# Kernel optimization log

Hardware: AMD Instinct MI355X
Metric: run time of the kernel (lower is better)

## Reference

```python
import jax, jax.numpy as jnp
import numpy as np

TOP_K = 2

def setup_inputs() -> dict:
    key = jax.random.key(0)
    ks = jax.random.split(key, 7)
    B, L, D, H, E, S = 2, 2048, 1024, 512, 16, 2048
    s = lambda fan_in: (1.0 / np.sqrt(fan_in)).astype(np.float32)
    return {
        "x": jax.random.normal(ks[0], (B, L, D), jnp.float32),
        "gate_w": jax.random.normal(ks[1], (E, D), jnp.float32) * s(D),
        "w1": jax.random.normal(ks[2], (E, H, D), jnp.float32) * s(D),
        "w2": jax.random.normal(ks[3], (E, D, H), jnp.float32) * s(H),
        "sfc1": jax.random.normal(ks[4], (S, D), jnp.float32) * s(D),
        "sfc2": jax.random.normal(ks[5], (S, D), jnp.float32) * s(D),
        "sfc3": jax.random.normal(ks[6], (D, S), jnp.float32) * s(S),
    }

def reference(x, gate_w, w1, w2, sfc1, sfc2, sfc3):
    B, L, D = x.shape
    E = gate_w.shape[0]
    # shared expert: SwiGLU MLP
    shared = jnp.einsum("bls,ds->bld", jax.nn.silu(jnp.einsum("bld,sd->bls", x, sfc1)) * jnp.einsum("bld,sd->bls", x, sfc2), sfc3)
    # router: top-k over gate logits, softmax over selected logits only
    logits = jnp.einsum("bld,ed->ble", x, gate_w)
    top_w, top_idx = jax.lax.top_k(logits, TOP_K)           # [B,L,K]
    top_w = jax.nn.softmax(top_w, axis=-1)
    xf = x.reshape(-1, D)                                    # [T,D]
    T = xf.shape[0]
    idx = top_idx.reshape(T, TOP_K)
    wk = top_w.reshape(T, TOP_K)
    # dense combine weights [T,E]: routing weight where selected, else 0
    dispatch = jnp.zeros((T, E), xf.dtype).at[jnp.arange(T)[:, None], idx].add(wk)
    # all-expert dense compute, combined with dispatch weights (avoids [T,E,D])
    h = jax.nn.silu(jnp.einsum("td,ehd->teh", xf, w1))       # [T,E,H]
    moe = jnp.einsum("teh,te,edh->td", h, dispatch, w2)      # [T,D]
    return moe.reshape(B, L, D) + shared
```

## Files before the change

kernel.cpp:

```cpp
#include <hip/hip_runtime.h>
#include <stdint.h>

#define T_TOK 4096
#define D_DIM 1024
#define H_DIM 512
#define E_NUM 16
#define S_DIM 2048

#define DUAL_BLOCKS 512
#define MOE1_TILES_MAX 80
#define SHOUT_BLOCKS 256

typedef __attribute__((ext_vector_type(8))) __bf16 bf16x8;
typedef __attribute__((ext_vector_type(16))) float f32x16;

__device__ __forceinline__ uint16_t f2bf(float f) {
  uint32_t u = __float_as_uint(f);
  u += 0x7fffu + ((u >> 16) & 1u);
  return (uint16_t)(u >> 16);
}

__device__ __forceinline__ float bf2f(uint16_t u) {
  return __uint_as_float(((uint32_t)u) << 16);
}

__device__ __forceinline__ float silu_f(float v) {
  return v / (1.f + __expf(-v));
}

#define N4_X (T_TOK * D_DIM / 4)
#define N4_S (S_DIM * D_DIM / 4)
#define N4_W (E_NUM * H_DIM * D_DIM / 4)
#define N4_TOT (N4_X + 3 * N4_S + 2 * N4_W)
#define N4_GW (E_NUM * D_DIM / 4)

__global__ __launch_bounds__(256) void k_cast_all(
    const float* __restrict__ x, const float* __restrict__ sfc1,
    const float* __restrict__ sfc2, const float* __restrict__ sfc3,
    const float* __restrict__ w1, const float* __restrict__ w2,
    const float* __restrict__ gw,
    uint16_t* __restrict__ xb, uint16_t* __restrict__ s1b,
    uint16_t* __restrict__ s2b, uint16_t* __restrict__ s3b,
    uint16_t* __restrict__ w1b, uint16_t* __restrict__ w2b,
    float4* __restrict__ gwT4) {
  int i = blockIdx.x * 256 + threadIdx.x;
  if (i >= N4_TOT) {
    int t = i - N4_TOT;
    if (t < N4_GW) {
      int k4 = t & (D_DIM / 4 - 1);
      int e = t >> 8;
      gwT4[(size_t)k4 * E_NUM + e] = ((const float4*)(gw + (size_t)e * D_DIM))[k4];
    }
    return;
  }
  const float* src; uint16_t* dst; int off;
  if (i < N4_X)                    { src = x;    dst = xb;  off = 0; }
  else if (i < N4_X + N4_S)        { src = sfc1; dst = s1b; off = N4_X; }
  else if (i < N4_X + 2 * N4_S)    { src = sfc2; dst = s2b; off = N4_X + N4_S; }
  else if (i < N4_X + 3 * N4_S)    { src = sfc3; dst = s3b; off = N4_X + 2 * N4_S; }
  else if (i < N4_X + 3 * N4_S + N4_W) { src = w1; dst = w1b; off = N4_X + 3 * N4_S; }
  else                             { src = w2;  dst = w2b; off = N4_X + 3 * N4_S + N4_W; }
  int j = i - off;
  float4 v = ((const float4*)src)[j];
  ushort4 o;
  o.x = f2bf(v.x); o.y = f2bf(v.y); o.z = f2bf(v.z); o.w = f2bf(v.w);
  ((ushort4*)dst)[j] = o;
}

__global__ __launch_bounds__(256) void k_router(
    const float* __restrict__ x, const float4* __restrict__ gwT4,
    int* __restrict__ top_idx, float* __restrict__ top_w) {
  const int wid = threadIdx.x >> 6, lane = threadIdx.x & 63;
  const int t = blockIdx.x * 4 + wid;
  const int e = lane & 15, q = lane >> 4;
  const float4* xr4 = (const float4*)(x + (size_t)t * D_DIM) + q * 64;
  const float4* g4 = gwT4 + (size_t)q * 64 * E_NUM + e;
  float acc = 0.f;
#pragma unroll 8
  for (int i = 0; i < 64; i++) {
    float4 xv = xr4[i];
    float4 gv = g4[(size_t)i * E_NUM];
    acc += xv.x * gv.x + xv.y * gv.y + xv.z * gv.z + xv.w * gv.w;
  }
  acc += __shfl_xor(acc, 16, 64);
  acc += __shfl_xor(acc, 32, 64);
  float v1 = acc; int i1 = e;
#pragma unroll
  for (int off = 1; off < 16; off <<= 1) {
    float ov = __shfl_xor(v1, off, 64);
    int oi = __shfl_xor(i1, off, 64);
    if (ov > v1 || (ov == v1 && oi < i1)) { v1 = ov; i1 = oi; }
  }
  float v2 = (e == i1) ? -1e30f : acc; int i2 = e;
#pragma unroll
  for (int off = 1; off < 16; off <<= 1) {
    float ov = __shfl_xor(v2, off, 64);
    int oi = __shfl_xor(i2, off, 64);
    if (ov > v2 || (ov == v2 && oi < i2)) { v2 = ov; i2 = oi; }
  }
  if (lane == 0) {
    float w0 = 1.f / (1.f + __expf(v2 - v1));
    top_idx[t * 2] = i1; top_idx[t * 2 + 1] = i2;
    top_w[t * 2] = w0;  top_w[t * 2 + 1] = 1.f - w0;
  }
}

__global__ __launch_bounds__(256) void k_sort(
    const int* __restrict__ top_idx, const float* __restrict__ top_w,
    int* __restrict__ offsets, int* __restrict__ tile_e,
    int* __restrict__ tile_m, int* __restrict__ tile_cnt,
    int* __restrict__ slot_token, float* __restrict__ slot_w,
    int* __restrict__ slot_of) {
  __shared__ int h[E_NUM];
  __shared__ int offs[E_NUM + 1];
  int tid = threadIdx.x;
  if (tid < E_NUM) h[tid] = 0;
  __syncthreads();
  for (int i = tid; i < 2 * T_TOK; i += 256) atomicAdd(&h[top_idx[i]], 1);
  __syncthreads();
  if (tid == 0) {
    int s = 0;
    for (int e = 0; e < E_NUM; e++) { offs[e] = s; s += h[e]; }
    offs[E_NUM] = s;
    int cnt = 0;
    for (int e = 0; e < E_NUM; e++)
      for (int m0 = 0; m0 < h[e]; m0 += 128) { tile_e[cnt] = e; tile_m[cnt] = m0; cnt++; }
    tile_cnt[0] = cnt;
    for (int e = 0; e <= E_NUM; e++) offsets[e] = offs[e];
  }
  __syncthreads();
  if (tid < E_NUM) h[tid] = offs[tid];
  __syncthreads();
  for (int i = tid; i < 2 * T_TOK; i += 256) {
    int e = top_idx[i];
    int slot = atomicAdd(&h[e], 1);
    slot_token[slot] = i >> 1;
    slot_w[slot] = top_w[i];
    slot_of[i] = slot;
  }
}


__global__ __launch_bounds__(256) void k_stage1(
    const uint16_t* __restrict__ xb, const uint16_t* __restrict__ b1,
    const uint16_t* __restrict__ b2, uint16_t* __restrict__ hs,
    const uint16_t* __restrict__ w1b, const int* __restrict__ offsets,
    const int* __restrict__ slot_token, const int* __restrict__ tile_e,
    const int* __restrict__ tile_m, const int* __restrict__ tile_cnt,
    uint16_t* __restrict__ hbuf) {
  __shared__ uint16_t smem[6 * 4096];
  const int bid = blockIdx.x;
  const int tid = threadIdx.x, lane = tid & 63, wid = tid >> 6;
  const int wm = wid >> 1, wn = wid & 1;
  const int m32 = lane & 31, kh = lane >> 5;
  const int row0 = tid >> 2, col8 = (tid & 3) * 8;
  const int st0 = tid * 8, st1 = 2048 + tid * 8;

  if (bid < DUAL_BLOCKS) {
    const int bn0 = (bid & 15) * 128, bm0 = (bid >> 4) * 128;
    uint16_t* sA = smem;
    uint16_t* sB1 = smem + 8192;
    uint16_t* sB2 = smem + 16384;
    f32x16 acc1[2][2], acc2[2][2];
#pragma unroll
    for (int i = 0; i < 2; i++)
#pragma unroll
      for (int j = 0; j < 2; j++) {
        acc1[i][j] = (f32x16)(0.f);
        acc2[i][j] = (f32x16)(0.f);
      }
    const uint16_t* ga0 = xb + (size_t)(bm0 + row0) * D_DIM + col8;
    const uint16_t* ga1 = ga0 + 64 * D_DIM;
    const uint16_t* gb10 = b1 + (size_t)(bn0 + row0) * D_DIM + col8;
    const uint16_t* gb11 = gb10 + 64 * D_DIM;
    const uint16_t* gb20 = b2 + (size_t)(bn0 + row0) * D_DIM + col8;
    const uint16_t* gb21 = gb20 + 64 * D_DIM;

    uint4 pA0, pA1, pB10, pB11, pB20, pB21;
    pA0 = *(const uint4*)ga0;   pA1 = *(const uint4*)ga1;
    pB10 = *(const uint4*)gb10; pB11 = *(const uint4*)gb11;
    pB20 = *(const uint4*)gb20; pB21 = *(const uint4*)gb21;
    ga0 += 32; ga1 += 32; gb10 += 32; gb11 += 32; gb20 += 32; gb21 += 32;
    *(uint4*)(sA + st0) = pA0;   *(uint4*)(sA + st1) = pA1;
    *(uint4*)(sB1 + st0) = pB10; *(uint4*)(sB1 + st1) = pB11;
    *(uint4*)(sB2 + st0) = pB20; *(uint4*)(sB2 + st1) = pB21;
    __syncthreads();

    int cur = 0;
    for (int kt = 32; kt <= D_DIM; kt += 32) {
      if (kt < D_DIM) {
        pA0 = *(const uint4*)ga0;   pA1 = *(const uint4*)ga1;
        pB10 = *(const uint4*)gb10; pB11 = *(const uint4*)gb11;
        pB20 = *(const uint4*)gb20; pB21 = *(const uint4*)gb21;
        ga0 += 32; ga1 += 32; gb10 += 32; gb11 += 32; gb20 += 32; gb21 += 32;
      }
      {
        const uint16_t* A = sA + cur * 4096;
        const uint16_t* B1 = sB1 + cur * 4096;
        const uint16_t* B2 = sB2 + cur * 4096;
#pragma unroll
        for (int ks = 0; ks < 2; ks++) {
          const int ko = ks * 16 + kh * 8;
          bf16x8 a[2], u[2], v[2];
#pragma unroll
          for (int i = 0; i < 2; i++)
            a[i] = *(const bf16x8*)(A + (wm * 64 + i * 32 + m32) * 32 + ko);
#pragma unroll
          for (int j = 0; j < 2; j++) {
            u[j] = *(const bf16x8*)(B1 + (wn * 64 + j * 32 + m32) * 32 + ko);
            v[j] = *(const bf16x8*)(B2 + (wn * 64 + j * 32 + m32) * 32 + ko);
          }
#pragma unroll
          for (int i = 0; i < 2; i++)
#pragma unroll
            for (int j = 0; j < 2; j++) {
              acc1[i][j] = __builtin_amdgcn_mfma_f32_32x32x16_bf16(a[i], u[j], acc1[i][j], 0, 0, 0);
              acc2[i][j] = __builtin_amdgcn_mfma_f32_32x32x16_bf16(a[i], v[j], acc2[i][j], 0, 0, 0);
            }
        }
      }
      if (kt < D_DIM) {
        int nxt = cur ^ 1;
        *(uint4*)(sA + nxt * 4096 + st0) = pA0;   *(uint4*)(sA + nxt * 4096 + st1) = pA1;
        *(uint4*)(sB1 + nxt * 4096 + st0) = pB10; *(uint4*)(sB1 + nxt * 4096 + st1) = pB11;
        *(uint4*)(sB2 + nxt * 4096 + st0) = pB20; *(uint4*)(sB2 + nxt * 4096 + st1) = pB21;
        __syncthreads();
        cur = nxt;
      }
    }
#pragma unroll
    for (int i = 0; i < 2; i++)
#pragma unroll
      for (int j = 0; j < 2; j++)
#pragma unroll
        for (int reg = 0; reg < 16; reg++) {
          int row = bm0 + wm * 64 + i * 32 + (reg & 3) + 8 * (reg >> 2) + 4 * kh;
          int col = bn0 + wn * 64 + j * 32 + m32;
          hs[(size_t)row * S_DIM + col] = f2bf(silu_f(acc1[i][j][reg]) * acc2[i][j][reg]);
        }
  } else {
    int idx = bid - DUAL_BLOCKS;
    int t = idx >> 2;
    if (t >= tile_cnt[0]) return;
    const int n0 = (idx & 3) * 128;
    const int e = tile_e[t], m0 = tile_m[t];
    const int base = offsets[e];
    const int ne = offsets[e + 1] - base;
    uint16_t* sA = smem;
    uint16_t* sB = smem + 8192;
    f32x16 acc[2][2];
#pragma unroll
    for (int i = 0; i < 2; i++)
#pragma unroll
      for (int j = 0; j < 2; j++) acc[i][j] = (f32x16)(0.f);
    const int e0 = min(m0 + row0, ne - 1);
    const int e1 = min(m0 + row0 + 64, ne - 1);
    const uint16_t* ga0 = xb + (size_t)slot_token[base + e0] * D_DIM + col8;
    const uint16_t* ga1 = xb + (size_t)slot_token[base + e1] * D_DIM + col8;
    const uint16_t* wbase = w1b + (size_t)e * H_DIM * D_DIM;
    const uint16_t* gb0 = wbase + (size_t)(n0 + row0) * D_DIM + col8;
    const uint16_t* gb1 = gb0 + 64 * D_DIM;

    uint4 pA0, pA1, pB0, pB1;
    pA0 = *(const uint4*)ga0; pA1 = *(const uint4*)ga1;
    pB0 = *(const uint4*)gb0; pB1 = *(const uint4*)gb1;
    ga0 += 32; ga1 += 32; gb0 += 32; gb1 += 32;
    *(uint4*)(sA + st0) = pA0; *(uint4*)(sA + st1) = pA1;
    *(uint4*)(sB + st0) = pB0; *(uint4*)(sB + st1) = pB1;
    __syncthreads();

    int cur = 0;
    for (int kt = 32; kt <= D_DIM; kt += 32) {
      if (kt < D_DIM) {
        pA0 = *(const uint4*)ga0; pA1 = *(const uint4*)ga1;
        pB0 = *(const uint4*)gb0; pB1 = *(const uint4*)gb1;
        ga0 += 32; ga1 += 32; gb0 += 32; gb1 += 32;
      }
      {
        const uint16_t* A = sA + cur * 4096;
        const uint16_t* B = sB + cur * 4096;
#pragma unroll
        for (int ks = 0; ks < 2; ks++) {
          const int ko = ks * 16 + kh * 8;
          bf16x8 a[2], bb[2];
#pragma unroll
          for (int i = 0; i < 2; i++)
            a[i] = *(const bf16x8*)(A + (wm * 64 + i * 32 + m32) * 32 + ko);
#pragma unroll
          for (int j = 0; j < 2; j++)
            bb[j] = *(const bf16x8*)(B + (wn * 64 + j * 32 + m32) * 32 + ko);
#pragma unroll
          for (int i = 0; i < 2; i++)
#pragma unroll
            for (int j = 0; j < 2; j++)
              acc[i][j] = __builtin_amdgcn_mfma_f32_32x32x16_bf16(a[i], bb[j], acc[i][j], 0, 0, 0);
        }
      }
      if (kt < D_DIM) {
        int nxt = cur ^ 1;
        *(uint4*)(sA + nxt * 4096 + st0) = pA0; *(uint4*)(sA + nxt * 4096 + st1) = pA1;
        *(uint4*)(sB + nxt * 4096 + st0) = pB0; *(uint4*)(sB + nxt * 4096 + st1) = pB1;
        __syncthreads();
        cur = nxt;
      }
    }
#pragma unroll
    for (int i = 0; i < 2; i++)
#pragma unroll
      for (int j = 0; j < 2; j++)
#pragma unroll
        for (int reg = 0; reg < 16; reg++) {
          int ent = m0 + wm * 64 + i * 32 + (reg & 3) + 8 * (reg >> 2) + 4 * kh;
          if (ent < ne) {
            int col = n0 + wn * 64 + j * 32 + m32;
            hbuf[(size_t)(base + ent) * H_DIM + col] = f2bf(silu_f(acc[i][j][reg]));
          }
        }
  }
}

__global__ __launch_bounds__(256) void k_stage2(
    const uint16_t* __restrict__ hsb, const uint16_t* __restrict__ sfc3b,
    float* __restrict__ out, const uint16_t* __restrict__ hbuf,
    const uint16_t* __restrict__ w2b, const int* __restrict__ offsets,
    const float* __restrict__ slot_w, const int* __restrict__ tile_e,
    const int* __restrict__ tile_m, const int* __restrict__ tile_cnt,
    uint16_t* __restrict__ slot_out) {
  __shared__ uint16_t smem[4 * 4096];
  const int bid = blockIdx.x;
  const int tid = threadIdx.x, lane = tid & 63, wid = tid >> 6;
  const int wm = wid >> 1, wn = wid & 1;
  const int m32 = lane & 31, kh = lane >> 5;
  const int row0 = tid >> 2, col8 = (tid & 3) * 8;
  const int st0 = tid * 8, st1 = 2048 + tid * 8;
  uint16_t* sA = smem;
  uint16_t* sB = smem + 8192;

  f32x16 acc[2][2];
#pragma unroll
  for (int i = 0; i < 2; i++)
#pragma unroll
    for (int j = 0; j < 2; j++) acc[i][j] = (f32x16)(0.f);

  const uint16_t *ga0, *ga1, *gb0, *gb1;
  int kiters;
  int bm0 = 0, bn0 = 0, base = 0, ne = 0, m0 = 0, n0 = 0;
  bool is_shout = (bid < SHOUT_BLOCKS);
  if (is_shout) {
    bn0 = (bid & 7) * 128; bm0 = (bid >> 3) * 128;
    ga0 = hsb + (size_t)(bm0 + row0) * S_DIM + col8;
    ga1 = ga0 + (size_t)64 * S_DIM;
    gb0 = sfc3b + (size_t)(bn0 + row0) * S_DIM + col8;
    gb1 = gb0 + (size_t)64 * S_DIM;
    kiters = S_DIM / 32;
  } else {
    int idx = bid - SHOUT_BLOCKS;
    int t = idx >> 3;
    if (t >= tile_cnt[0]) return;
    n0 = (idx & 7) * 128;
    int e = tile_e[t]; m0 = tile_m[t];
    base = offsets[e];
    ne = offsets[e + 1] - base;
    const int e0 = min(m0 + row0, ne - 1);
    const int e1 = min(m0 + row0 + 64, ne - 1);
    ga0 = hbuf + (size_t)(base + e0) * H_DIM + col8;
    ga1 = hbuf + (size_t)(base + e1) * H_DIM + col8;
    const uint16_t* wbase = w2b + (size_t)e * D_DIM * H_DIM;
    gb0 = wbase + (size_t)(n0 + row0) * H_DIM + col8;
    gb1 = gb0 + 64 * H_DIM;
    kiters = H_DIM / 32;
  }

  uint4 pA0, pA1, pB0, pB1;
  pA0 = *(const uint4*)ga0; pA1 = *(const uint4*)ga1;
  pB0 = *(const uint4*)gb0; pB1 = *(const uint4*)gb1;
  ga0 += 32; ga1 += 32; gb0 += 32; gb1 += 32;
  *(uint4*)(sA + st0) = pA0; *(uint4*)(sA + st1) = pA1;
  *(uint4*)(sB + st0) = pB0; *(uint4*)(sB + st1) = pB1;
  __syncthreads();

  int cur = 0;
  for (int kt = 1; kt <= kiters; kt++) {
    if (kt < kiters) {
      pA0 = *(const uint4*)ga0; pA1 = *(const uint4*)ga1;
      pB0 = *(const uint4*)gb0; pB1 = *(const uint4*)gb1;
      ga0 += 32; ga1 += 32; gb0 += 32; gb1 += 32;
    }
    {
      const uint16_t* A = sA + cur * 4096;
      const uint16_t* B = sB + cur * 4096;
#pragma unroll
      for (int ks = 0; ks < 2; ks++) {
        const int ko = ks * 16 + kh * 8;
        bf16x8 a[2], bb[2];
#pragma unroll
        for (int i = 0; i < 2; i++)
          a[i] = *(const bf16x8*)(A + (wm * 64 + i * 32 + m32) * 32 + ko);
#pragma unroll
        for (int j = 0; j < 2; j++)
          bb[j] = *(const bf16x8*)(B + (wn * 64 + j * 32 + m32) * 32 + ko);
#pragma unroll
        for (int i = 0; i < 2; i++)
#pragma unroll
          for (int j = 0; j < 2; j++)
            acc[i][j] = __builtin_amdgcn_mfma_f32_32x32x16_bf16(a[i], bb[j], acc[i][j], 0, 0, 0);
      }
    }
    if (kt < kiters) {
      int nxt = cur ^ 1;
      *(uint4*)(sA + nxt * 4096 + st0) = pA0; *(uint4*)(sA + nxt * 4096 + st1) = pA1;
      *(uint4*)(sB + nxt * 4096 + st0) = pB0; *(uint4*)(sB + nxt * 4096 + st1) = pB1;
      __syncthreads();
      cur = nxt;
    }
  }

  if (is_shout) {
#pragma unroll
    for (int i = 0; i < 2; i++)
#pragma unroll
      for (int j = 0; j < 2; j++)
#pragma unroll
        for (int reg = 0; reg < 16; reg++) {
          int row = bm0 + wm * 64 + i * 32 + (reg & 3) + 8 * (reg >> 2) + 4 * kh;
          int col = bn0 + wn * 64 + j * 32 + m32;
          out[(size_t)row * D_DIM + col] = acc[i][j][reg];
        }
  } else {
#pragma unroll
    for (int i = 0; i < 2; i++)
#pragma unroll
      for (int reg = 0; reg < 16; reg++) {
        int ent = m0 + wm * 64 + i * 32 + (reg & 3) + 8 * (reg >> 2) + 4 * kh;
        if (ent < ne) {
          float w = slot_w[base + ent];
          uint16_t* orow = slot_out + (size_t)(base + ent) * D_DIM;
#pragma unroll
          for (int j = 0; j < 2; j++) {
            int col = n0 + wn * 64 + j * 32 + m32;
            orow[col] = f2bf(w * acc[i][j][reg]);
          }
        }
      }
  }
}

__global__ __launch_bounds__(256) void k_combine(
    const uint16_t* __restrict__ slot_out, const int* __restrict__ slot_of,
    float* __restrict__ out) {
  int t = blockIdx.x;
  int c = threadIdx.x;
  int s0 = slot_of[t * 2], s1 = slot_of[t * 2 + 1];
  ushort4 a = ((const ushort4*)(slot_out + (size_t)s0 * D_DIM))[c];
  ushort4 b = ((const ushort4*)(slot_out + (size_t)s1 * D_DIM))[c];
  float4* po = (float4*)(out + (size_t)t * D_DIM) + c;
  float4 o = *po;
  o.x += bf2f(a.x) + bf2f(b.x);
  o.y += bf2f(a.y) + bf2f(b.y);
  o.z += bf2f(a.z) + bf2f(b.z);
  o.w += bf2f(a.w) + bf2f(b.w);
  *po = o;
}

extern "C" void kernel_launch(void* const* d_in, const int* in_sizes, int n_in,
                              void* d_out, int out_size, void* d_ws, size_t ws_size,
                              hipStream_t stream) {
  const float* x     = (const float*)d_in[0];
  const float* gatew = (const float*)d_in[1];
  const float* w1    = (const float*)d_in[2];
  const float* w2    = (const float*)d_in[3];
  const float* sfc1  = (const float*)d_in[4];
  const float* sfc2  = (const float*)d_in[5];
  const float* sfc3  = (const float*)d_in[6];
  float* out = (float*)d_out;

  uint8_t* ws = (uint8_t*)d_ws;
  size_t off = 0;
  auto alloc = [&](size_t bytes) {
    void* p = ws + off;
    off = (off + bytes + 255) & ~(size_t)255;
    return p;
  };
  uint16_t* xb    = (uint16_t*)alloc((size_t)T_TOK * D_DIM * 2);
  uint16_t* sfc1b = (uint16_t*)alloc((size_t)S_DIM * D_DIM * 2);
  uint16_t* sfc2b = (uint16_t*)alloc((size_t)S_DIM * D_DIM * 2);
  uint16_t* sfc3b = (uint16_t*)alloc((size_t)D_DIM * S_DIM * 2);
  uint16_t* w1b   = (uint16_t*)alloc((size_t)E_NUM * H_DIM * D_DIM * 2);
  uint16_t* w2b   = (uint16_t*)alloc((size_t)E_NUM * D_DIM * H_DIM * 2);
  uint16_t* hsb   = (uint16_t*)alloc((size_t)T_TOK * S_DIM * 2);
  uint16_t* hbuf  = (uint16_t*)alloc((size_t)2 * T_TOK * H_DIM * 2);
  uint16_t* slot_out = (uint16_t*)alloc((size_t)2 * T_TOK * D_DIM * 2);
  float4* gwT4    = (float4*)alloc((size_t)D_DIM / 4 * E_NUM * 16);
  int*   top_idx  = (int*)alloc((size_t)T_TOK * 2 * 4);
  float* top_w    = (float*)alloc((size_t)T_TOK * 2 * 4);
  int*   offsets  = (int*)alloc((E_NUM + 1) * 4);
  int*   tile_e   = (int*)alloc(MOE1_TILES_MAX * 4);
  int*   tile_m   = (int*)alloc(MOE1_TILES_MAX * 4);
  int*   tile_cnt = (int*)alloc(4);
  int*   slot_token = (int*)alloc((size_t)2 * T_TOK * 4);
  float* slot_w   = (float*)alloc((size_t)2 * T_TOK * 4);
  int*   slot_of  = (int*)alloc((size_t)2 * T_TOK * 4);

  k_cast_all<<<(N4_TOT + N4_GW + 255) / 256, 256, 0, stream>>>(
      x, sfc1, sfc2, sfc3, w1, w2, gatew,
      xb, sfc1b, sfc2b, sfc3b, w1b, w2b, gwT4);
  k_router<<<T_TOK / 4, 256, 0, stream>>>(x, gwT4, top_idx, top_w);
  k_sort<<<1, 256, 0, stream>>>(top_idx, top_w, offsets, tile_e, tile_m,
                                tile_cnt, slot_token, slot_w, slot_of);
  k_stage1<<<DUAL_BLOCKS + MOE1_TILES_MAX * 4, 256, 0, stream>>>(
      xb, sfc1b, sfc2b, hsb, w1b, offsets, slot_token, tile_e, tile_m, tile_cnt, hbuf);
  k_stage2<<<SHOUT_BLOCKS + MOE1_TILES_MAX * 8, 256, 0, stream>>>(
      hsb, sfc3b, out, hbuf, w2b, offsets, slot_w, tile_e, tile_m, tile_cnt, slot_out);
  k_combine<<<T_TOK, 256, 0, stream>>>(slot_out, slot_of, out);
}
```

Measured before the change: 354.8 us.

## Switch GEMMs to 16x16x32 MFMA, defer sfc3/w2 casts into stage1, reorder tiles

```diff
diff --git a/kernel.cpp b/kernel.cpp
--- a/kernel.cpp
+++ b/kernel.cpp
@@ -7,12 +7,13 @@
 #define E_NUM 16
 #define S_DIM 2048
 
+#define CAST2_BLOCKS 256
 #define DUAL_BLOCKS 512
 #define MOE1_TILES_MAX 80
 #define SHOUT_BLOCKS 256
 
 typedef __attribute__((ext_vector_type(8))) __bf16 bf16x8;
-typedef __attribute__((ext_vector_type(16))) float f32x16;
+typedef __attribute__((ext_vector_type(4))) float f32x4;
 
 __device__ __forceinline__ uint16_t f2bf(float f) {
   uint32_t u = __float_as_uint(f);
@@ -31,21 +32,20 @@
 #define N4_X (T_TOK * D_DIM / 4)
 #define N4_S (S_DIM * D_DIM / 4)
 #define N4_W (E_NUM * H_DIM * D_DIM / 4)
-#define N4_TOT (N4_X + 3 * N4_S + 2 * N4_W)
+#define N4_P1 (N4_X + 2 * N4_S + N4_W)
 #define N4_GW (E_NUM * D_DIM / 4)
-
-__global__ __launch_bounds__(256) void k_cast_all(
+#define N4_P2 (N4_S + N4_W)
+
+__global__ __launch_bounds__(256) void k_cast1(
     const float* __restrict__ x, const float* __restrict__ sfc1,
-    const float* __restrict__ sfc2, const float* __restrict__ sfc3,
-    const float* __restrict__ w1, const float* __restrict__ w2,
+    const float* __restrict__ sfc2, const float* __restrict__ w1,
     const float* __restrict__ gw,
     uint16_t* __restrict__ xb, uint16_t* __restrict__ s1b,
-    uint16_t* __restrict__ s2b, uint16_t* __restrict__ s3b,
-    uint16_t* __restrict__ w1b, uint16_t* __restrict__ w2b,
+    uint16_t* __restrict__ s2b, uint16_t* __restrict__ w1b,
     float4* __restrict__ gwT4) {
   int i = blockIdx.x * 256 + threadIdx.x;
-  if (i >= N4_TOT) {
-    int t = i - N4_TOT;
+  if (i >= N4_P1) {
+    int t = i - N4_P1;
     if (t < N4_GW) {
       int k4 = t & (D_DIM / 4 - 1);
       int e = t >> 8;
@@ -54,12 +54,10 @@
     return;
   }
   const float* src; uint16_t* dst; int off;
-  if (i < N4_X)                    { src = x;    dst = xb;  off = 0; }
-  else if (i < N4_X + N4_S)        { src = sfc1; dst = s1b; off = N4_X; }
-  else if (i < N4_X + 2 * N4_S)    { src = sfc2; dst = s2b; off = N4_X + N4_S; }
-  else if (i < N4_X + 3 * N4_S)    { src = sfc3; dst = s3b; off = N4_X + 2 * N4_S; }
-  else if (i < N4_X + 3 * N4_S + N4_W) { src = w1; dst = w1b; off = N4_X + 3 * N4_S; }
-  else                             { src = w2;  dst = w2b; off = N4_X + 3 * N4_S + N4_W; }
+  if (i < N4_X)                  { src = x;    dst = xb;  off = 0; }
+  else if (i < N4_X + N4_S)      { src = sfc1; dst = s1b; off = N4_X; }
+  else if (i < N4_X + 2 * N4_S)  { src = sfc2; dst = s2b; off = N4_X + N4_S; }
+  else                           { src = w1;   dst = w1b; off = N4_X + 2 * N4_S; }
   int j = i - off;
   float4 v = ((const float4*)src)[j];
   ushort4 o;
@@ -140,34 +138,49 @@
   }
 }
 
-
 __global__ __launch_bounds__(256) void k_stage1(
     const uint16_t* __restrict__ xb, const uint16_t* __restrict__ b1,
     const uint16_t* __restrict__ b2, uint16_t* __restrict__ hs,
     const uint16_t* __restrict__ w1b, const int* __restrict__ offsets,
     const int* __restrict__ slot_token, const int* __restrict__ tile_e,
     const int* __restrict__ tile_m, const int* __restrict__ tile_cnt,
-    uint16_t* __restrict__ hbuf) {
+    uint16_t* __restrict__ hbuf,
+    const float* __restrict__ sfc3, const float* __restrict__ w2,
+    uint16_t* __restrict__ s3b, uint16_t* __restrict__ w2b) {
   __shared__ uint16_t smem[6 * 4096];
   const int bid = blockIdx.x;
   const int tid = threadIdx.x, lane = tid & 63, wid = tid >> 6;
   const int wm = wid >> 1, wn = wid & 1;
-  const int m32 = lane & 31, kh = lane >> 5;
+  const int r = lane & 15, q = lane >> 4;
   const int row0 = tid >> 2, col8 = (tid & 3) * 8;
   const int st0 = tid * 8, st1 = 2048 + tid * 8;
 
-  if (bid < DUAL_BLOCKS) {
-    const int bn0 = (bid & 15) * 128, bm0 = (bid >> 4) * 128;
+  if (bid < CAST2_BLOCKS) {
+    for (int i = bid * 256 + tid; i < N4_P2; i += CAST2_BLOCKS * 256) {
+      const float* src; uint16_t* dst; int j;
+      if (i < N4_S) { src = sfc3; dst = s3b; j = i; }
+      else          { src = w2;   dst = w2b; j = i - N4_S; }
+      float4 v = ((const float4*)src)[j];
+      ushort4 o;
+      o.x = f2bf(v.x); o.y = f2bf(v.y); o.z = f2bf(v.z); o.w = f2bf(v.w);
+      ((ushort4*)dst)[j] = o;
+    }
+    return;
+  }
+
+  if (bid < CAST2_BLOCKS + DUAL_BLOCKS) {
+    const int b = bid - CAST2_BLOCKS;
+    const int bm0 = (b & 31) * 128, bn0 = (b >> 5) * 128;
     uint16_t* sA = smem;
     uint16_t* sB1 = smem + 8192;
     uint16_t* sB2 = smem + 16384;
-    f32x16 acc1[2][2], acc2[2][2];
-#pragma unroll
-    for (int i = 0; i < 2; i++)
-#pragma unroll
-      for (int j = 0; j < 2; j++) {
-        acc1[i][j] = (f32x16)(0.f);
-        acc2[i][j] = (f32x16)(0.f);
+    f32x4 acc1[4][4], acc2[4][4];
+#pragma unroll
+    for (int i = 0; i < 4; i++)
+#pragma unroll
+      for (int j = 0; j < 4; j++) {
+        acc1[i][j] = (f32x4){0.f, 0.f, 0.f, 0.f};
+        acc2[i][j] = (f32x4){0.f, 0.f, 0.f, 0.f};
       }
     const uint16_t* ga0 = xb + (size_t)(bm0 + row0) * D_DIM + col8;
     const uint16_t* ga1 = ga0 + 64 * D_DIM;
@@ -187,59 +200,76 @@
     __syncthreads();
 
     int cur = 0;
-    for (int kt = 32; kt <= D_DIM; kt += 32) {
-      if (kt < D_DIM) {
-        pA0 = *(const uint4*)ga0;   pA1 = *(const uint4*)ga1;
-        pB10 = *(const uint4*)gb10; pB11 = *(const uint4*)gb11;
-        pB20 = *(const uint4*)gb20; pB21 = *(const uint4*)gb21;
-        ga0 += 32; ga1 += 32; gb10 += 32; gb11 += 32; gb20 += 32; gb21 += 32;
-      }
+    for (int kt = 32; kt < D_DIM; kt += 32) {
+      pA0 = *(const uint4*)ga0;   pA1 = *(const uint4*)ga1;
+      pB10 = *(const uint4*)gb10; pB11 = *(const uint4*)gb11;
+      pB20 = *(const uint4*)gb20; pB21 = *(const uint4*)gb21;
+      ga0 += 32; ga1 += 32; gb10 += 32; gb11 += 32; gb20 += 32; gb21 += 32;
       {
         const uint16_t* A = sA + cur * 4096;
         const uint16_t* B1 = sB1 + cur * 4096;
         const uint16_t* B2 = sB2 + cur * 4096;
-#pragma unroll
-        for (int ks = 0; ks < 2; ks++) {
-          const int ko = ks * 16 + kh * 8;
-          bf16x8 a[2], u[2], v[2];
-#pragma unroll
-          for (int i = 0; i < 2; i++)
-            a[i] = *(const bf16x8*)(A + (wm * 64 + i * 32 + m32) * 32 + ko);
-#pragma unroll
-          for (int j = 0; j < 2; j++) {
-            u[j] = *(const bf16x8*)(B1 + (wn * 64 + j * 32 + m32) * 32 + ko);
-            v[j] = *(const bf16x8*)(B2 + (wn * 64 + j * 32 + m32) * 32 + ko);
-          }
-#pragma unroll
-          for (int i = 0; i < 2; i++)
-#pragma unroll
-            for (int j = 0; j < 2; j++) {
-              acc1[i][j] = __builtin_amdgcn_mfma_f32_32x32x16_bf16(a[i], u[j], acc1[i][j], 0, 0, 0);
-              acc2[i][j] = __builtin_amdgcn_mfma_f32_32x32x16_bf16(a[i], v[j], acc2[i][j], 0, 0, 0);
-            }
+        bf16x8 a[4];
+#pragma unroll
+        for (int i = 0; i < 4; i++)
+          a[i] = *(const bf16x8*)(A + (wm * 64 + i * 16 + r) * 32 + q * 8);
+#pragma unroll
+        for (int j = 0; j < 4; j++) {
+          bf16x8 b = *(const bf16x8*)(B1 + (wn * 64 + j * 16 + r) * 32 + q * 8);
+#pragma unroll
+          for (int i = 0; i < 4; i++)
+            acc1[i][j] = __builtin_amdgcn_mfma_f32_16x16x32_bf16(a[i], b, acc1[i][j], 0, 0, 0);
+        }
+#pragma unroll
+        for (int j = 0; j < 4; j++) {
+          bf16x8 b = *(const bf16x8*)(B2 + (wn * 64 + j * 16 + r) * 32 + q * 8);
+#pragma unroll
+          for (int i = 0; i < 4; i++)
+            acc2[i][j] = __builtin_amdgcn_mfma_f32_16x16x32_bf16(a[i], b, acc2[i][j], 0, 0, 0);
         }
       }
-      if (kt < D_DIM) {
-        int nxt = cur ^ 1;
-        *(uint4*)(sA + nxt * 4096 + st0) = pA0;   *(uint4*)(sA + nxt * 4096 + st1) = pA1;
-        *(uint4*)(sB1 + nxt * 4096 + st0) = pB10; *(uint4*)(sB1 + nxt * 4096 + st1) = pB11;
-        *(uint4*)(sB2 + nxt * 4096 + st0) = pB20; *(uint4*)(sB2 + nxt * 4096 + st1) = pB21;
-        __syncthreads();
-        cur = nxt;
+      int nxt = cur ^ 1;
+      *(uint4*)(sA + nxt * 4096 + st0) = pA0;   *(uint4*)(sA + nxt * 4096 + st1) = pA1;
+      *(uint4*)(sB1 + nxt * 4096 + st0) = pB10; *(uint4*)(sB1 + nxt * 4096 + st1) = pB11;
+      *(uint4*)(sB2 + nxt * 4096 + st0) = pB20; *(uint4*)(sB2 + nxt * 4096 + st1) = pB21;
+      __syncthreads();
+      cur = nxt;
+    }
+    {
+      const uint16_t* A = sA + cur * 4096;
+      const uint16_t* B1 = sB1 + cur * 4096;
+      const uint16_t* B2 = sB2 + cur * 4096;
+      bf16x8 a[4];
+#pragma unroll
+      for (int i = 0; i < 4; i++)
+        a[i] = *(const bf16x8*)(A + (wm * 64 + i * 16 + r) * 32 + q * 8);
+#pragma unroll
+      for (int j = 0; j < 4; j++) {
+        bf16x8 b = *(const bf16x8*)(B1 + (wn * 64 + j * 16 + r) * 32 + q * 8);
+#pragma unroll
+        for (int i = 0; i < 4; i++)
+          acc1[i][j] = __builtin_amdgcn_mfma_f32_16x16x32_bf16(a[i], b, acc1[i][j], 0, 0, 0);
       }
-    }
-#pragma unroll
-    for (int i = 0; i < 2; i++)
-#pragma unroll
-      for (int j = 0; j < 2; j++)
-#pragma unroll
-        for (int reg = 0; reg < 16; reg++) {
-          int row = bm0 + wm * 64 + i * 32 + (reg & 3) + 8 * (reg >> 2) + 4 * kh;
-          int col = bn0 + wn * 64 + j * 32 + m32;
-          hs[(size_t)row * S_DIM + col] = f2bf(silu_f(acc1[i][j][reg]) * acc2[i][j][reg]);
+#pragma unroll
+      for (int j = 0; j < 4; j++) {
+        bf16x8 b = *(const bf16x8*)(B2 + (wn * 64 + j * 16 + r) * 32 + q * 8);
+#pragma unroll
+        for (int i = 0; i < 4; i++)
+          acc2[i][j] = __builtin_amdgcn_mfma_f32_16x16x32_bf16(a[i], b, acc2[i][j], 0, 0, 0);
+      }
+    }
+#pragma unroll
+    for (int i = 0; i < 4; i++)
+#pragma unroll
+      for (int j = 0; j < 4; j++)
+#pragma unroll
+        for (int rr = 0; rr < 4; rr++) {
+          int row = bm0 + wm * 64 + i * 16 + q * 4 + rr;
+          int col = bn0 + wn * 64 + j * 16 + r;
+          hs[(size_t)row * S_DIM + col] = f2bf(silu_f(acc1[i][j][rr]) * acc2[i][j][rr]);
         }
   } else {
-    int idx = bid - DUAL_BLOCKS;
+    int idx = bid - CAST2_BLOCKS - DUAL_BLOCKS;
     int t = idx >> 2;
     if (t >= tile_cnt[0]) return;
     const int n0 = (idx & 3) * 128;
@@ -248,11 +278,11 @@
     const int ne = offsets[e + 1] - base;
     uint16_t* sA = smem;
     uint16_t* sB = smem + 8192;
-    f32x16 acc[2][2];
-#pragma unroll
-    for (int i = 0; i < 2; i++)
-#pragma unroll
-      for (int j = 0; j < 2; j++) acc[i][j] = (f32x16)(0.f);
+    f32x4 acc[4][4];
+#pragma unroll
+    for (int i = 0; i < 4; i++)
+#pragma unroll
+      for (int j = 0; j < 4; j++) acc[i][j] = (f32x4){0.f, 0.f, 0.f, 0.f};
     const int e0 = min(m0 + row0, ne - 1);
     const int e1 = min(m0 + row0 + 64, ne - 1);
     const uint16_t* ga0 = xb + (size_t)slot_token[base + e0] * D_DIM + col8;
@@ -270,50 +300,58 @@
     __syncthreads();
 
     int cur = 0;
-    for (int kt = 32; kt <= D_DIM; kt += 32) {
-      if (kt < D_DIM) {
-        pA0 = *(const uint4*)ga0; pA1 = *(const uint4*)ga1;
-        pB0 = *(const uint4*)gb0; pB1 = *(const uint4*)gb1;
-        ga0 += 32; ga1 += 32; gb0 += 32; gb1 += 32;
-      }
+    for (int kt = 32; kt < D_DIM; kt += 32) {
+      pA0 = *(const uint4*)ga0; pA1 = *(const uint4*)ga1;
+      pB0 = *(const uint4*)gb0; pB1 = *(const uint4*)gb1;
+      ga0 += 32; ga1 += 32; gb0 += 32; gb1 += 32;
       {
         const uint16_t* A = sA + cur * 4096;
         const uint16_t* B = sB + cur * 4096;
-#pragma unroll
-        for (int ks = 0; ks < 2; ks++) {
-          const int ko = ks * 16 + kh * 8;
-          bf16x8 a[2], bb[2];
-#pragma unroll
-          for (int i = 0; i < 2; i++)
-            a[i] = *(const bf16x8*)(A + (wm * 64 + i * 32 + m32) * 32 + ko);
-#pragma unroll
-          for (int j = 0; j < 2; j++)
-            bb[j] = *(const bf16x8*)(B + (wn * 64 + j * 32 + m32) * 32 + ko);
-#pragma unroll
-          for (int i = 0; i < 2; i++)
-#pragma unroll
-            for (int j = 0; j < 2; j++)
-              acc[i][j] = __builtin_amdgcn_mfma_f32_32x32x16_bf16(a[i], bb[j], acc[i][j], 0, 0, 0);
-        }
+        bf16x8 a[4], bb[4];
+#pragma unroll
+        for (int i = 0; i < 4; i++)
+          a[i] = *(const bf16x8*)(A + (wm * 64 + i * 16 + r) * 32 + q * 8);
+#pragma unroll
+        for (int j = 0; j < 4; j++)
+          bb[j] = *(const bf16x8*)(B + (wn * 64 + j * 16 + r) * 32 + q * 8);
+#pragma unroll
+        for (int i = 0; i < 4; i++)
+#pragma unroll
+          for (int j = 0; j < 4; j++)
+            acc[i][j] = __builtin_amdgcn_mfma_f32_16x16x32_bf16(a[i], bb[j], acc[i][j], 0, 0, 0);
       }
-      if (kt < D_DIM) {
-        int nxt = cur ^ 1;
-        *(uint4*)(sA + nxt * 4096 + st0) = pA0; *(uint4*)(sA + nxt * 4096 + st1) = pA1;
-        *(uint4*)(sB + nxt * 4096 + st0) = pB0; *(uint4*)(sB + nxt * 4096 + st1) = pB1;
-        __syncthreads();
-        cur = nxt;
-      }
-    }
-#pragma unroll
-    for (int i = 0; i < 2; i++)
-#pragma unroll
-      for (int j = 0; j < 2; j++)
-#pragma unroll
-        for (int reg = 0; reg < 16; reg++) {
-          int ent = m0 + wm * 64 + i * 32 + (reg & 3) + 8 * (reg >> 2) + 4 * kh;
+      int nxt = cur ^ 1;
+      *(uint4*)(sA + nxt * 4096 + st0) = pA0; *(uint4*)(sA + nxt * 4096 + st1) = pA1;
+      *(uint4*)(sB + nxt * 4096 + st0) = pB0; *(uint4*)(sB + nxt * 4096 + st1) = pB1;
+      __syncthreads();
+      cur = nxt;
+    }
+    {
+      const uint16_t* A = sA + cur * 4096;
+      const uint16_t* B = sB + cur * 4096;
+      bf16x8 a[4], bb[4];
+#pragma unroll
+      for (int i = 0; i < 4; i++)
+        a[i] = *(const bf16x8*)(A + (wm * 64 + i * 16 + r) * 32 + q * 8);
+#pragma unroll
+      for (int j = 0; j < 4; j++)
+        bb[j] = *(const bf16x8*)(B + (wn * 64 + j * 16 + r) * 32 + q * 8);
+#pragma unroll
+      for (int i = 0; i < 4; i++)
+#pragma unroll
+        for (int j = 0; j < 4; j++)
+          acc[i][j] = __builtin_amdgcn_mfma_f32_16x16x32_bf16(a[i], bb[j], acc[i][j], 0, 0, 0);
+    }
+#pragma unroll
+    for (int i = 0; i < 4; i++)
+#pragma unroll
+      for (int j = 0; j < 4; j++)
+#pragma unroll
+        for (int rr = 0; rr < 4; rr++) {
+          int ent = m0 + wm * 64 + i * 16 + q * 4 + rr;
           if (ent < ne) {
-            int col = n0 + wn * 64 + j * 32 + m32;
-            hbuf[(size_t)(base + ent) * H_DIM + col] = f2bf(silu_f(acc[i][j][reg]));
+            int col = n0 + wn * 64 + j * 16 + r;
+            hbuf[(size_t)(base + ent) * H_DIM + col] = f2bf(silu_f(acc[i][j][rr]));
           }
         }
   }
@@ -330,24 +368,24 @@
   const int bid = blockIdx.x;
   const int tid = threadIdx.x, lane = tid & 63, wid = tid >> 6;
   const int wm = wid >> 1, wn = wid & 1;
-  const int m32 = lane & 31, kh = lane >> 5;
+  const int r = lane & 15, q = lane >> 4;
   const int row0 = tid >> 2, col8 = (tid & 3) * 8;
   const int st0 = tid * 8, st1 = 2048 + tid * 8;
   uint16_t* sA = smem;
   uint16_t* sB = smem + 8192;
 
-  f32x16 acc[2][2];
-#pragma unroll
-  for (int i = 0; i < 2; i++)
-#pragma unroll
-    for (int j = 0; j < 2; j++) acc[i][j] = (f32x16)(0.f);
+  f32x4 acc[4][4];
+#pragma unroll
+  for (int i = 0; i < 4; i++)
+#pragma unroll
+    for (int j = 0; j < 4; j++) acc[i][j] = (f32x4){0.f, 0.f, 0.f, 0.f};
 
   const uint16_t *ga0, *ga1, *gb0, *gb1;
   int kiters;
   int bm0 = 0, bn0 = 0, base = 0, ne = 0, m0 = 0, n0 = 0;
   bool is_shout = (bid < SHOUT_BLOCKS);
   if (is_shout) {
-    bn0 = (bid & 7) * 128; bm0 = (bid >> 3) * 128;
+    bm0 = (bid & 31) * 128; bn0 = (bid >> 5) * 128;
     ga0 = hsb + (size_t)(bm0 + row0) * S_DIM + col8;
     ga1 = ga0 + (size_t)64 * S_DIM;
     gb0 = sfc3b + (size_t)(bn0 + row0) * S_DIM + col8;
@@ -389,22 +427,18 @@
     {
       const uint16_t* A = sA + cur * 4096;
       const uint16_t* B = sB + cur * 4096;
-#pragma unroll
-      for (int ks = 0; ks < 2; ks++) {
-        const int ko = ks * 16 + kh * 8;
-        bf16x8 a[2], bb[2];
-#pragma unroll
-        for (int i = 0; i < 2; i++)
-          a[i] = *(const bf16x8*)(A + (wm * 64 + i * 32 + m32) * 32 + ko);
-#pragma unroll
-        for (int j = 0; j < 2; j++)
-          bb[j] = *(const bf16x8*)(B + (wn * 64 + j * 32 + m32) * 32 + ko);
-#pragma unroll
-        for (int i = 0; i < 2; i++)
-#pragma unroll
-          for (int j = 0; j < 2; j++)
-            acc[i][j] = __builtin_amdgcn_mfma_f32_32x32x16_bf16(a[i], bb[j], acc[i][j], 0, 0, 0);
-      }
+      bf16x8 a[4], bb[4];
+#pragma unroll
+      for (int i = 0; i < 4; i++)
+        a[i] = *(const bf16x8*)(A + (wm * 64 + i * 16 + r) * 32 + q * 8);
+#pragma unroll
+      for (int j = 0; j < 4; j++)
+        bb[j] = *(const bf16x8*)(B + (wn * 64 + j * 16 + r) * 32 + q * 8);
+#pragma unroll
+      for (int i = 0; i < 4; i++)
+#pragma unroll
+        for (int j = 0; j < 4; j++)
+          acc[i][j] = __builtin_amdgcn_mfma_f32_16x16x32_bf16(a[i], bb[j], acc[i][j], 0, 0, 0);
     }
     if (kt < kiters) {
       int nxt = cur ^ 1;
@@ -417,31 +451,33 @@
 
   if (is_shout) {
 #pragma unroll
-    for (int i = 0; i < 2; i++)
-#pragma unroll
-      for (int j = 0; j < 2; j++)
-#pragma unroll
-        for (int reg = 0; reg < 16; reg++) {
-          int row = bm0 + wm * 64 + i * 32 + (reg & 3) + 8 * (reg >> 2) + 4 * kh;
-          int col = bn0 + wn * 64 + j * 32 + m32;
-          out[(size_t)row * D_DIM + col] = acc[i][j][reg];
+    for (int i = 0; i < 4; i++)
+#pragma unroll
+      for (int j = 0; j < 4; j++)
+#pragma unroll
+        for (int rr = 0; rr < 4; rr++) {
+          int row = bm0 + wm * 64 + i * 16 + q * 4 + rr;
+          int col = bn0 + wn * 64 + j * 16 + r;
+          out[(size_t)row * D_DIM + col] = acc[i][j][rr];
         }
   } else {
 #pragma unroll
-    for (int i = 0; i < 2; i++)
-#pragma unroll
-      for (int reg = 0; reg < 16; reg++) {
-        int ent = m0 + wm * 64 + i * 32 + (reg & 3) + 8 * (reg >> 2) + 4 * kh;
+    for (int i = 0; i < 4; i++) {
+      int ent_base = m0 + wm * 64 + i * 16 + q * 4;
+#pragma unroll
+      for (int rr = 0; rr < 4; rr++) {
+        int ent = ent_base + rr;
         if (ent < ne) {
           float w = slot_w[base + ent];
           uint16_t* orow = slot_out + (size_t)(base + ent) * D_DIM;
 #pragma unroll
-          for (int j = 0; j < 2; j++) {
-            int col = n0 + wn * 64 + j * 32 + m32;
-            orow[col] = f2bf(w * acc[i][j][reg]);
+          for (int j = 0; j < 4; j++) {
+            int col = n0 + wn * 64 + j * 16 + r;
+            orow[col] = f2bf(w * acc[i][j][rr]);
           }
         }
       }
+    }
   }
 }
 
@@ -501,14 +537,14 @@
   float* slot_w   = (float*)alloc((size_t)2 * T_TOK * 4);
   int*   slot_of  = (int*)alloc((size_t)2 * T_TOK * 4);
 
-  k_cast_all<<<(N4_TOT + N4_GW + 255) / 256, 256, 0, stream>>>(
-      x, sfc1, sfc2, sfc3, w1, w2, gatew,
-      xb, sfc1b, sfc2b, sfc3b, w1b, w2b, gwT4);
+  k_cast1<<<(N4_P1 + N4_GW + 255) / 256, 256, 0, stream>>>(
+      x, sfc1, sfc2, w1, gatew, xb, sfc1b, sfc2b, w1b, gwT4);
   k_router<<<T_TOK / 4, 256, 0, stream>>>(x, gwT4, top_idx, top_w);
   k_sort<<<1, 256, 0, stream>>>(top_idx, top_w, offsets, tile_e, tile_m,
                                 tile_cnt, slot_token, slot_w, slot_of);
-  k_stage1<<<DUAL_BLOCKS + MOE1_TILES_MAX * 4, 256, 0, stream>>>(
-      xb, sfc1b, sfc2b, hsb, w1b, offsets, slot_token, tile_e, tile_m, tile_cnt, hbuf);
+  k_stage1<<<CAST2_BLOCKS + DUAL_BLOCKS + MOE1_TILES_MAX * 4, 256, 0, stream>>>(
+      xb, sfc1b, sfc2b, hsb, w1b, offsets, slot_token, tile_e, tile_m, tile_cnt,
+      hbuf, sfc3, w2, sfc3b, w2b);
   k_stage2<<<SHOUT_BLOCKS + MOE1_TILES_MAX * 8, 256, 0, stream>>>(
       hsb, sfc3b, out, hbuf, w2b, offsets, slot_w, tile_e, tile_m, tile_cnt, slot_out);
   k_combine<<<T_TOK, 256, 0, stream>>>(slot_out, slot_of, out);
```

New measurement: 317.5 us. 1.12x faster.
